# Kernel tuning notes

Measured on AMD Instinct MI355X. Metric: run time of the kernel, lower is better.

The kernel has to match this reference:

```python
import jax, jax.numpy as jnp
import numpy as np

NQ = 8
NL = 6
DIM = 2 ** NQ
C64 = jnp.complex64
I2 = jnp.eye(2, dtype=C64)
PX = jnp.array([[0., 1.], [1., 0.]], dtype=C64)
PY = jnp.array([[0., -1j], [1j, 0.]], dtype=C64)
PZ = jnp.array([[1., 0.], [0., -1.]], dtype=C64)
# sign of Pauli-Z eigenvalue for each computational basis state, wires 0..3 (wire 0 = MSB)
_idx = np.arange(DIM)
_SIGNS = jnp.asarray(np.stack([1.0 - 2.0 * ((_idx >> (NQ - 1 - w)) & 1) for w in range(4)]).astype(np.float32))  # (4, 256)

def _rot(t, P):
    # exp(-i t/2 P) = cos(t/2) I - i sin(t/2) P
    th = t.astype(jnp.float32) / 2
    return jnp.cos(th) * I2 - 1j * jnp.sin(th) * P

def _apply1(st, U, w):
    # apply 2x2 unitary U on wire w; st: (B, 2,2,...,2)
    s = jnp.moveaxis(st, w + 1, -1)
    return jnp.moveaxis(s @ U.T, -1, w + 1)

def _cnot(st, c, t):
    # flip target axis where control bit == 1
    s = jnp.moveaxis(st, (c + 1, t + 1), (1, 2))
    s = jnp.concatenate([s[:, :1], s[:, 1:, ::-1]], axis=1)
    return jnp.moveaxis(s, (1, 2), (c + 1, t + 1))

def _quantum(x, weights):
    B = x.shape[0]
    # AmplitudeEmbedding with normalize=True
    psi = (x / jnp.linalg.norm(x, axis=1, keepdims=True)).astype(C64)
    st = psi.reshape((B,) + (2,) * NQ)
    for l in range(NL):
        lw = weights[l]
        for q in range(NQ):
            st = _apply1(st, _rot(lw[3 * q], PX), q)
            st = _apply1(st, _rot(lw[3 * q + 1], PY), q)
            st = _apply1(st, _rot(lw[3 * q + 2], PZ), q)
        for i in range(NQ - 1):
            st = _cnot(st, i, i + 1)
        st = _cnot(st, NQ - 1, 0)
        for i in range(0, NQ, 2):
            if i + 2 < NQ:
                st = _cnot(st, i, i + 2)
    probs = jnp.abs(st.reshape(B, DIM)) ** 2
    return probs @ _SIGNS.T  # (B, 4) Z expectations on wires 0..3

def _bn(h, g, b):
    # BatchNorm1d, training mode (batch statistics, biased variance)
    m = h.mean(0)
    v = h.var(0)
    return g * (h - m) * jax.lax.rsqrt(v + 1e-5) + b

def _forward(x, q_weights, aW, ab, fW1, fb1, fW2, fb2, cW1, cb1, g1, be1, cW2, cb2, g2, be2, cW3, cb3, cW4, cb4):
    q = _quantum(x, q_weights)                     # (B, 4)
    qf = q @ aW.T + ab                             # quantum_adapter
    cf = jnp.tanh(jax.nn.relu(x @ fW1.T + fb1) @ fW2.T + fb2)  # feature_processor
    h = qf + cf
    h = jax.nn.relu(_bn(h @ cW1.T + cb1, g1, be1))
    h = jax.nn.relu(_bn(h @ cW2.T + cb2, g2, be2))
    h = jax.nn.relu(h @ cW3.T + cb3)
    return jax.nn.sigmoid(h @ cW4.T + cb4)         # (B, 1)

def setup_inputs():
    key = jax.random.key(0)
    ks = jax.random.split(key, 21)
    f32 = jnp.float32
    r = lambda k, shp, s: jax.random.normal(k, shp, dtype=f32) * s
    B = 8192
    return {
        'x': r(ks[0], (B, 256), 1.0),
        'q_weights': r(ks[1], (NL, NQ * 3), 1.0),
        'aW': r(ks[2], (4, 4), 0.5), 'ab': r(ks[3], (4,), 0.1),
        'fW1': r(ks[4], (64, 256), 0.0625), 'fb1': r(ks[5], (64,), 0.05),
        'fW2': r(ks[6], (4, 64), 0.125), 'fb2': r(ks[7], (4,), 0.05),
        'cW1': r(ks[8], (32, 4), 0.5), 'cb1': r(ks[9], (32,), 0.05),
        'g1': 1.0 + r(ks[10], (32,), 0.05), 'be1': r(ks[11], (32,), 0.05),
        'cW2': r(ks[12], (16, 32), 0.18), 'cb2': r(ks[13], (16,), 0.05),
        'g2': 1.0 + r(ks[14], (16,), 0.05), 'be2': r(ks[15], (16,), 0.05),
        'cW3': r(ks[16], (8, 16), 0.25), 'cb3': r(ks[17], (8,), 0.05),
        'cW4': r(ks[18], (1, 8), 0.35), 'cb4': r(ks[19], (1,), 0.05),
    }

def reference(x, q_weights, aW, ab, fW1, fb1, fW2, fb2, cW1, cb1, g1, be1, cW2, cb2, g2, be2, cW3, cb3, cW4, cb4):
    return _forward(x, q_weights, aW, ab, fW1, fb1, fW2, fb2, cW1, cb1, g1, be1, cW2, cb2, g2, be2, cW3, cb3, cW4, cb4)
```

## Files before the change

kernel.cpp:

```cpp
#include <hip/hip_runtime.h>
#include <math.h>

#define INV_B (1.0f / 8192.0f)

typedef float  v2f  __attribute__((ext_vector_type(2)));
typedef _Float16 half8 __attribute__((ext_vector_type(8)));
typedef float  f32x4 __attribute__((ext_vector_type(4)));

struct QTables {
    int xm[6][8];
    int rm[6][8];
    int meas[4];
};
constexpr QTables make_tables() {
    QTables T{};
    int Mrow[8] = {}, Ncol[8] = {};
    for (int b = 0; b < 8; ++b) { Mrow[b] = 1 << b; Ncol[b] = 1 << b; }
    constexpr int bc[11] = {7,6,5,4,3,2,1,0,7,5,3};
    constexpr int bt[11] = {6,5,4,3,2,1,0,7,5,3,1};
    for (int l = 0; l < 6; ++l) {
        for (int w = 0; w < 8; ++w) { T.xm[l][w] = Ncol[7 - w]; T.rm[l][w] = Mrow[7 - w]; }
        for (int k = 0; k < 11; ++k) { Mrow[bt[k]] ^= Mrow[bc[k]]; Ncol[bc[k]] ^= Ncol[bt[k]]; }
    }
    for (int w = 0; w < 4; ++w) T.meas[w] = Mrow[7 - w];
    return T;
}
constexpr QTables TB = make_tables();

template<int ML>
static __device__ __forceinline__ float lanex(float v) {
    if constexpr (ML == 0) { return v; }
    else if constexpr (ML == 1) { return __int_as_float(__builtin_amdgcn_update_dpp(0, __float_as_int(v), 0xB1, 0xF, 0xF, true)); }
    else if constexpr (ML == 2) { return __int_as_float(__builtin_amdgcn_update_dpp(0, __float_as_int(v), 0x4E, 0xF, 0xF, true)); }
    else if constexpr (ML == 3) { return __int_as_float(__builtin_amdgcn_update_dpp(0, __float_as_int(v), 0x1B, 0xF, 0xF, true)); }
    else if constexpr (ML < 32) { return __int_as_float(__builtin_amdgcn_ds_swizzle(__float_as_int(v), 0x1F | (ML << 10))); }
    else { return __shfl_xor(v, ML, 64); }
}

static __device__ __forceinline__ float bsum64(float v) {
    v += lanex<1>(v);  v += lanex<2>(v);
    v += lanex<4>(v);  v += lanex<8>(v);
    v += lanex<16>(v); v += __shfl_xor(v, 32, 64);
    return v;
}

static __device__ __forceinline__ float tanh_fast(float v) {
    const float c = fminf(fmaxf(v, -10.f), 10.f);
    const float e = __expf(2.f * c);
    return (e - 1.f) / (e + 1.f);
}

template<int XM, int RM>
static __device__ __forceinline__ void gate(v2f (&z)[4], const int lane,
                                            const float u00r, const float u00i,
                                            const float u01r, const float u01i) {
    constexpr int ML = XM >> 2, MR = XM & 3;
    constexpr int RL = RM >> 2, RR = RM & 3;
    const int pl = __popc(lane & RL) & 1;
    const float csi0 = pl ? -u00i : u00i;
    const float cpr0 = pl ? -u01r : u01r;
    const float csi1 = -csi0, cpr1 = -cpr0;
    v2f p[4];
    #pragma unroll
    for (int r = 0; r < 4; ++r) {
        p[r].x = lanex<ML>(z[r ^ MR].x);
        p[r].y = lanex<ML>(z[r ^ MR].y);
    }
    #pragma unroll
    for (int r = 0; r < 4; ++r) {
        const int pb = __builtin_popcount(r & RR) & 1;
        const float csi = pb ? csi1 : csi0;
        const float cpr = pb ? cpr1 : cpr0;
        const v2f zs = { -z[r].y, z[r].x };
        const v2f ps = { -p[r].y, p[r].x };
        z[r] = ((u00r * z[r] + csi * zs) + cpr * p[r]) + u01i * ps;
    }
}

#define XS 264
__global__ __launch_bounds__(256) void k_feat(
        const float* __restrict__ x, const float* __restrict__ qw,
        const float* __restrict__ fW1, const float* __restrict__ fb1,
        const float* __restrict__ fW2, const float* __restrict__ fb2,
        float* __restrict__ U, float* __restrict__ cfws, float* __restrict__ accz) {
    const int t = threadIdx.x, b = blockIdx.x;

    if (t < 16) accz[b * 16 + t] = 0.f;
    if (b == 0 && t < 48) {
        const int l = t >> 3, q = t & 7;
        const float* a = qw + l * 24 + q * 3;
        const float h1 = 0.5f * a[0], h2 = 0.5f * a[1], h3 = 0.5f * a[2];
        const float c1 = cosf(h1), s1 = sinf(h1);
        const float c2 = cosf(h2), s2 = sinf(h2);
        const float c3 = cosf(h3), s3 = sinf(h3);
        const float m00r =  c1 * c2, m00i =  s1 * s2;
        const float m01r = -c1 * s2, m01i = -s1 * c2;
        float4 u;
        u.x = m00r * c3 + m00i * s3;  u.y = m00i * c3 - m00r * s3;
        u.z = m01r * c3 + m01i * s3;  u.w = m01i * c3 - m01r * s3;
        ((float4*)U)[t] = u;
    }

    __shared__ _Float16 xl[64 * XS];
    __shared__ _Float16 wl[64 * XS];
    const long r0 = (long)b * 64;
    #pragma unroll
    for (int i = 0; i < 16; ++i) {
        const int idx = i * 256 + t;
        const int row = idx >> 6, c4 = idx & 63;
        const float4 xv = ((const float4*)(x + (r0 + row) * 256))[c4];
        _Float16* d = &xl[row * XS + c4 * 4];
        d[0] = (_Float16)xv.x; d[1] = (_Float16)xv.y;
        d[2] = (_Float16)xv.z; d[3] = (_Float16)xv.w;
        const float4 wv = ((const float4*)(fW1 + (long)row * 256))[c4];
        _Float16* e = &wl[row * XS + c4 * 4];
        e[0] = (_Float16)wv.x; e[1] = (_Float16)wv.y;
        e[2] = (_Float16)wv.z; e[3] = (_Float16)wv.w;
    }
    __syncthreads();

    const int lane = t & 63, w4 = t >> 6;
    const int g = lane >> 4, col = lane & 15;
    const int rloc = w4 * 16 + col;

    half8 bf[8];
    #pragma unroll
    for (int kb = 0; kb < 8; ++kb)
        bf[kb] = *(const half8*)&xl[rloc * XS + kb * 32 + g * 8];

    float accc[4] = {0.f, 0.f, 0.f, 0.f};
    #pragma unroll
    for (int jc = 0; jc < 4; ++jc) {
        f32x4 cv = {0.f, 0.f, 0.f, 0.f};
        #pragma unroll
        for (int kb = 0; kb < 8; ++kb) {
            const half8 af = *(const half8*)&wl[(jc * 16 + col) * XS + kb * 32 + g * 8];
            cv = __builtin_amdgcn_mfma_f32_16x16x32_f16(af, bf[kb], cv, 0, 0, 0);
        }
        #pragma unroll
        for (int r = 0; r < 4; ++r) {
            const int j = jc * 16 + g * 4 + r;
            const float z = fmaxf(cv[r] + fb1[j], 0.f);
            #pragma unroll
            for (int c = 0; c < 4; ++c) accc[c] += z * fW2[c * 64 + j];
        }
    }
    #pragma unroll
    for (int c = 0; c < 4; ++c) {
        accc[c] += __shfl_xor(accc[c], 16, 64);
        accc[c] += __shfl_xor(accc[c], 32, 64);
    }
    if (g == 0) {
        float4 o;
        o.x = tanh_fast(accc[0] + fb2[0]);
        o.y = tanh_fast(accc[1] + fb2[1]);
        o.z = tanh_fast(accc[2] + fb2[2]);
        o.w = tanh_fast(accc[3] + fb2[3]);
        ((float4*)cfws)[r0 + w4 * 16 + col] = o;
    }
}

__global__ __launch_bounds__(256) void k_main(
        const float* __restrict__ x, const float* __restrict__ U,
        const float* __restrict__ cfws,
        const float* __restrict__ aW, const float* __restrict__ ab,
        float* __restrict__ hws, float* __restrict__ acc1) {
    const int t = threadIdx.x, lane = t & 63, wv = t >> 6;
    const int b = blockIdx.x;
    const int row = b * 4 + wv;

    const float4 xr = ((const float4*)(x + (long)row * 256))[lane];

    v2f z[4] = { {xr.x, 0.f}, {xr.y, 0.f}, {xr.z, 0.f}, {xr.w, 0.f} };
    const float4* U4 = (const float4*)U;

#define GATE(L, W) { const float4 u = U4[(L) * 8 + (W)]; \
                     gate<TB.xm[L][W], TB.rm[L][W]>(z, lane, u.x, u.y, u.z, u.w); }
#define LAYER(L) GATE(L,0) GATE(L,1) GATE(L,2) GATE(L,3) GATE(L,4) GATE(L,5) GATE(L,6) GATE(L,7)
    LAYER(0) LAYER(1) LAYER(2) LAYER(3) LAYER(4) LAYER(5)
#undef LAYER
#undef GATE

    float pv[4];
    #pragma unroll
    for (int r = 0; r < 4; ++r) pv[r] = z[r].x * z[r].x + z[r].y * z[r].y;
    float S = pv[0] + pv[1] + pv[2] + pv[3];
    float qs[4];
    #pragma unroll
    for (int w = 0; w < 4; ++w) {
        const int mm = TB.meas[w];
        const int plm = __popc(lane & (mm >> 2)) & 1;
        float s = 0.f;
        #pragma unroll
        for (int r = 0; r < 4; ++r) {
            const int sgn = plm ^ (__builtin_popcount(r & (mm & 3)) & 1);
            s += sgn ? -pv[r] : pv[r];
        }
        qs[w] = s;
    }
    S = bsum64(S);
    const float inv = 1.0f / S;
    float qe[4];
    #pragma unroll
    for (int w = 0; w < 4; ++w) qe[w] = bsum64(qs[w]) * inv;

    const float4 cfv = ((const float4*)cfws)[row];
    const float cf[4] = {cfv.x, cfv.y, cfv.z, cfv.w};
    float h[4];
    #pragma unroll
    for (int k = 0; k < 4; ++k) {
        float s = ab[k] + cf[k];
        #pragma unroll
        for (int j = 0; j < 4; ++j) s += aW[k * 4 + j] * qe[j];
        h[k] = s;
    }
    if (lane == 0)
        ((float4*)hws)[row] = make_float4(h[0], h[1], h[2], h[3]);

    __shared__ float wsum[4][20];
    if (lane == 0) {
        #pragma unroll
        for (int k = 0; k < 4; ++k) wsum[wv][k] = h[k];
        #pragma unroll
        for (int j = 0; j < 4; ++j)
            #pragma unroll
            for (int k = 0; k < 4; ++k) wsum[wv][4 + j * 4 + k] = h[j] * h[k];
    }
    __syncthreads();
    if (t < 20)
        atomicAdd(acc1 + (b & 31) * 20 + t,
                  wsum[0][t] + wsum[1][t] + wsum[2][t] + wsum[3][t]);
}

__global__ __launch_bounds__(64) void k_mid(
        const float* __restrict__ hws, const float* __restrict__ acc1,
        const float* __restrict__ cW1, const float* __restrict__ cb1,
        const float* __restrict__ g1, const float* __restrict__ be1,
        const float* __restrict__ cW2, const float* __restrict__ cb2,
        float* __restrict__ z2ws, float* __restrict__ acc2) {
    const int t = threadIdx.x;
    __shared__ float sA[20];
    __shared__ float m1s[32], is1[32];
    if (t < 20) {
        float s = 0.f;
        for (int sl = 0; sl < 32; ++sl) s += acc1[sl * 20 + t];
        sA[t] = s;
    }
    __syncthreads();
    if (t < 32) {
        float mu[4], w[4];
        #pragma unroll
        for (int k = 0; k < 4; ++k) mu[k] = sA[k] * INV_B;
        float m = cb1[t];
        #pragma unroll
        for (int k = 0; k < 4; ++k) { w[k] = cW1[t * 4 + k]; m += w[k] * mu[k]; }
        float var = 0.f;
        #pragma unroll
        for (int a2 = 0; a2 < 4; ++a2)
            #pragma unroll
            for (int b2 = 0; b2 < 4; ++b2)
                var += w[a2] * w[b2] * (sA[4 + a2 * 4 + b2] * INV_B - mu[a2] * mu[b2]);
        m1s[t] = m;
        is1[t] = 1.0f / sqrtf(var + 1e-5f);
    }
    __syncthreads();

    const long e = (long)blockIdx.x * 64 + t;
    const float4 h4 = ((const float4*)hws)[e];
    const float h[4] = {h4.x, h4.y, h4.z, h4.w};
    float a1[32];
    #pragma unroll
    for (int j = 0; j < 32; ++j) {
        float zz = cb1[j];
        #pragma unroll
        for (int k = 0; k < 4; ++k) zz += cW1[j * 4 + k] * h[k];
        a1[j] = fmaxf((zz - m1s[j]) * is1[j] * g1[j] + be1[j], 0.f);
    }
    float z2[16];
    #pragma unroll
    for (int k = 0; k < 16; ++k) {
        float s = cb2[k];
        #pragma unroll
        for (int j = 0; j < 32; ++j) s += cW2[k * 32 + j] * a1[j];
        z2[k] = s;
    }
    float4* zp = (float4*)(z2ws + e * 16);
    zp[0] = make_float4(z2[0], z2[1], z2[2], z2[3]);
    zp[1] = make_float4(z2[4], z2[5], z2[6], z2[7]);
    zp[2] = make_float4(z2[8], z2[9], z2[10], z2[11]);
    zp[3] = make_float4(z2[12], z2[13], z2[14], z2[15]);

    float sv[16], sq[16];
    #pragma unroll
    for (int k = 0; k < 16; ++k) { sv[k] = z2[k]; sq[k] = z2[k] * z2[k]; }
    #pragma unroll
    for (int m = 1; m < 64; m <<= 1) {
        #pragma unroll
        for (int k = 0; k < 16; ++k) {
            sv[k] += __shfl_xor(sv[k], m, 64);
            sq[k] += __shfl_xor(sq[k], m, 64);
        }
    }
    if (t == 0) {
        float* dst = acc2 + (blockIdx.x & 31) * 32;
        #pragma unroll
        for (int k = 0; k < 16; ++k) atomicAdd(dst + k, sv[k]);
        #pragma unroll
        for (int k = 0; k < 16; ++k) atomicAdd(dst + 16 + k, sq[k]);
    }
}

__global__ __launch_bounds__(64) void k_out(
        const float* __restrict__ z2ws, const float* __restrict__ acc2,
        const float* __restrict__ g2, const float* __restrict__ be2,
        const float* __restrict__ cW3, const float* __restrict__ cb3,
        const float* __restrict__ cW4, const float* __restrict__ cb4,
        float* __restrict__ out) {
    const int t = threadIdx.x;
    __shared__ float sB[32];
    __shared__ float m2s[16], is2[16];
    if (t < 32) {
        float s = 0.f;
        for (int sl = 0; sl < 32; ++sl) s += acc2[sl * 32 + t];
        sB[t] = s;
    }
    __syncthreads();
    if (t < 16) {
        const float m = sB[t] * INV_B;
        const float var = sB[16 + t] * INV_B - m * m;
        m2s[t] = m;
        is2[t] = 1.0f / sqrtf(var + 1e-5f);
    }
    __syncthreads();

    const long e = (long)blockIdx.x * 64 + t;
    const float4* zp = (const float4*)(z2ws + e * 16);
    const float4 v0 = zp[0], v1 = zp[1], v2 = zp[2], v3 = zp[3];
    const float z2[16] = {v0.x, v0.y, v0.z, v0.w, v1.x, v1.y, v1.z, v1.w,
                          v2.x, v2.y, v2.z, v2.w, v3.x, v3.y, v3.z, v3.w};
    float a2[16];
    #pragma unroll
    for (int k = 0; k < 16; ++k)
        a2[k] = fmaxf((z2[k] - m2s[k]) * is2[k] * g2[k] + be2[k], 0.f);
    float z3[8];
    #pragma unroll
    for (int j = 0; j < 8; ++j) {
        float s = cb3[j];
        #pragma unroll
        for (int k = 0; k < 16; ++k) s += cW3[j * 16 + k] * a2[k];
        z3[j] = fmaxf(s, 0.f);
    }
    float y = cb4[0];
    #pragma unroll
    for (int j = 0; j < 8; ++j) y += cW4[j] * z3[j];
    out[e] = 1.0f / (1.0f + expf(-y));
}

extern "C" void kernel_launch(void* const* d_in, const int* in_sizes, int n_in,
                              void* d_out, int out_size, void* d_ws, size_t ws_size,
                              hipStream_t stream) {
    (void)in_sizes; (void)n_in; (void)out_size; (void)ws_size;
    const float* x   = (const float*)d_in[0];
    const float* qw  = (const float*)d_in[1];
    const float* aW  = (const float*)d_in[2];
    const float* ab  = (const float*)d_in[3];
    const float* fW1 = (const float*)d_in[4];
    const float* fb1 = (const float*)d_in[5];
    const float* fW2 = (const float*)d_in[6];
    const float* fb2 = (const float*)d_in[7];
    const float* cW1 = (const float*)d_in[8];
    const float* cb1 = (const float*)d_in[9];
    const float* g1  = (const float*)d_in[10];
    const float* be1 = (const float*)d_in[11];
    const float* cW2 = (const float*)d_in[12];
    const float* cb2 = (const float*)d_in[13];
    const float* g2  = (const float*)d_in[14];
    const float* be2 = (const float*)d_in[15];
    const float* cW3 = (const float*)d_in[16];
    const float* cb3 = (const float*)d_in[17];
    const float* cW4 = (const float*)d_in[18];
    const float* cb4 = (const float*)d_in[19];

    float* ws   = (float*)d_ws;
    float* acc1 = ws;
    float* acc2 = ws + 1024;
    float* U    = ws + 2048;
    float* cfws = ws + 4096;
    float* hws  = ws + 40960;
    float* z2ws = ws + 81920;

    k_feat<<<128, 256, 0, stream>>>(x, qw, fW1, fb1, fW2, fb2, U, cfws, ws);
    k_main<<<2048, 256, 0, stream>>>(x, U, cfws, aW, ab, hws, acc1);
    k_mid <<<128, 64, 0, stream>>>(hws, acc1, cW1, cb1, g1, be1, cW2, cb2, z2ws, acc2);
    k_out <<<128, 64, 0, stream>>>(z2ws, acc2, g2, be2, cW3, cb3, cW4, cb4, (float*)d_out);
}
```

Measured before the change: 148.1 us.

## Process two state rows per wave and fuse the BatchNorm tail kernels with a grid barrier

The quantum-simulation kernel now carries two batch rows per wavefront, eight complex registers per lane, so each gate's cross-lane exchanges and FMAs for two independent states interleave. This adds instruction-level parallelism and halves the grid. The last two small kernels are merged into one, using an atomic counter spin barrier across the 128 blocks to get the second BatchNorm statistics. That drops a launch and the z2 workspace round-trip, but relies on all blocks being co-resident.

Result: slower. 151.7 us (+2.4%).

```diff
diff --git a/kernel.cpp b/kernel.cpp
--- a/kernel.cpp
+++ b/kernel.cpp
@@ -51,29 +51,30 @@
 }
 
 template<int XM, int RM>
-static __device__ __forceinline__ void gate(v2f (&z)[4], const int lane,
-                                            const float u00r, const float u00i,
-                                            const float u01r, const float u01i) {
+static __device__ __forceinline__ void gate2(v2f (&z)[8], const int lane,
+                                             const float u00r, const float u00i,
+                                             const float u01r, const float u01i) {
     constexpr int ML = XM >> 2, MR = XM & 3;
     constexpr int RL = RM >> 2, RR = RM & 3;
     const int pl = __popc(lane & RL) & 1;
     const float csi0 = pl ? -u00i : u00i;
     const float cpr0 = pl ? -u01r : u01r;
     const float csi1 = -csi0, cpr1 = -cpr0;
-    v2f p[4];
-    #pragma unroll
-    for (int r = 0; r < 4; ++r) {
-        p[r].x = lanex<ML>(z[r ^ MR].x);
-        p[r].y = lanex<ML>(z[r ^ MR].y);
-    }
-    #pragma unroll
-    for (int r = 0; r < 4; ++r) {
-        const int pb = __builtin_popcount(r & RR) & 1;
+    v2f p[8];
+    #pragma unroll
+    for (int rr = 0; rr < 8; ++rr) {
+        const int src = (rr & 4) | ((rr & 3) ^ MR);
+        p[rr].x = lanex<ML>(z[src].x);
+        p[rr].y = lanex<ML>(z[src].y);
+    }
+    #pragma unroll
+    for (int rr = 0; rr < 8; ++rr) {
+        const int pb = __builtin_popcount(rr & RR) & 1;
         const float csi = pb ? csi1 : csi0;
         const float cpr = pb ? cpr1 : cpr0;
-        const v2f zs = { -z[r].y, z[r].x };
-        const v2f ps = { -p[r].y, p[r].x };
-        z[r] = ((u00r * z[r] + csi * zs) + cpr * p[r]) + u01i * ps;
+        const v2f zs = { -z[rr].y, z[rr].x };
+        const v2f ps = { -p[rr].y, p[rr].x };
+        z[rr] = ((u00r * z[rr] + csi * zs) + cpr * p[rr]) + u01i * ps;
     }
 }
 
@@ -167,77 +168,94 @@
         float* __restrict__ hws, float* __restrict__ acc1) {
     const int t = threadIdx.x, lane = t & 63, wv = t >> 6;
     const int b = blockIdx.x;
-    const int row = b * 4 + wv;
-
-    const float4 xr = ((const float4*)(x + (long)row * 256))[lane];
-
-    v2f z[4] = { {xr.x, 0.f}, {xr.y, 0.f}, {xr.z, 0.f}, {xr.w, 0.f} };
+    const int rowA = b * 8 + wv * 2, rowB = rowA + 1;
+
+    const float4 xa = ((const float4*)(x + (long)rowA * 256))[lane];
+    const float4 xb = ((const float4*)(x + (long)rowB * 256))[lane];
+    const float4 cfa = ((const float4*)cfws)[rowA];
+    const float4 cfb = ((const float4*)cfws)[rowB];
+
+    v2f z[8] = { {xa.x, 0.f}, {xa.y, 0.f}, {xa.z, 0.f}, {xa.w, 0.f},
+                 {xb.x, 0.f}, {xb.y, 0.f}, {xb.z, 0.f}, {xb.w, 0.f} };
     const float4* U4 = (const float4*)U;
 
 #define GATE(L, W) { const float4 u = U4[(L) * 8 + (W)]; \
-                     gate<TB.xm[L][W], TB.rm[L][W]>(z, lane, u.x, u.y, u.z, u.w); }
+                     gate2<TB.xm[L][W], TB.rm[L][W]>(z, lane, u.x, u.y, u.z, u.w); }
 #define LAYER(L) GATE(L,0) GATE(L,1) GATE(L,2) GATE(L,3) GATE(L,4) GATE(L,5) GATE(L,6) GATE(L,7)
     LAYER(0) LAYER(1) LAYER(2) LAYER(3) LAYER(4) LAYER(5)
 #undef LAYER
 #undef GATE
 
-    float pv[4];
-    #pragma unroll
-    for (int r = 0; r < 4; ++r) pv[r] = z[r].x * z[r].x + z[r].y * z[r].y;
-    float S = pv[0] + pv[1] + pv[2] + pv[3];
-    float qs[4];
-    #pragma unroll
-    for (int w = 0; w < 4; ++w) {
-        const int mm = TB.meas[w];
-        const int plm = __popc(lane & (mm >> 2)) & 1;
-        float s = 0.f;
+    float hA[4], hB[4];
+    #pragma unroll
+    for (int half = 0; half < 2; ++half) {
+        float pv[4];
         #pragma unroll
         for (int r = 0; r < 4; ++r) {
-            const int sgn = plm ^ (__builtin_popcount(r & (mm & 3)) & 1);
-            s += sgn ? -pv[r] : pv[r];
-        }
-        qs[w] = s;
-    }
-    S = bsum64(S);
-    const float inv = 1.0f / S;
-    float qe[4];
-    #pragma unroll
-    for (int w = 0; w < 4; ++w) qe[w] = bsum64(qs[w]) * inv;
-
-    const float4 cfv = ((const float4*)cfws)[row];
-    const float cf[4] = {cfv.x, cfv.y, cfv.z, cfv.w};
-    float h[4];
-    #pragma unroll
-    for (int k = 0; k < 4; ++k) {
-        float s = ab[k] + cf[k];
-        #pragma unroll
-        for (int j = 0; j < 4; ++j) s += aW[k * 4 + j] * qe[j];
-        h[k] = s;
-    }
-    if (lane == 0)
-        ((float4*)hws)[row] = make_float4(h[0], h[1], h[2], h[3]);
-
-    __shared__ float wsum[4][20];
+            const v2f zz = z[half * 4 + r];
+            pv[r] = zz.x * zz.x + zz.y * zz.y;
+        }
+        float S = pv[0] + pv[1] + pv[2] + pv[3];
+        float qs[4];
+        #pragma unroll
+        for (int w = 0; w < 4; ++w) {
+            const int mm = TB.meas[w];
+            const int plm = __popc(lane & (mm >> 2)) & 1;
+            float s = 0.f;
+            #pragma unroll
+            for (int r = 0; r < 4; ++r) {
+                const int sgn = plm ^ (__builtin_popcount(r & (mm & 3)) & 1);
+                s += sgn ? -pv[r] : pv[r];
+            }
+            qs[w] = s;
+        }
+        S = bsum64(S);
+        const float inv = 1.0f / S;
+        float qe[4];
+        #pragma unroll
+        for (int w = 0; w < 4; ++w) qe[w] = bsum64(qs[w]) * inv;
+
+        const float4 cfv = half ? cfb : cfa;
+        const float cf[4] = {cfv.x, cfv.y, cfv.z, cfv.w};
+        float* h = half ? hB : hA;
+        #pragma unroll
+        for (int k = 0; k < 4; ++k) {
+            float s = ab[k] + cf[k];
+            #pragma unroll
+            for (int j = 0; j < 4; ++j) s += aW[k * 4 + j] * qe[j];
+            h[k] = s;
+        }
+    }
     if (lane == 0) {
-        #pragma unroll
-        for (int k = 0; k < 4; ++k) wsum[wv][k] = h[k];
-        #pragma unroll
-        for (int j = 0; j < 4; ++j)
-            #pragma unroll
-            for (int k = 0; k < 4; ++k) wsum[wv][4 + j * 4 + k] = h[j] * h[k];
-    }
-    __syncthreads();
-    if (t < 20)
-        atomicAdd(acc1 + (b & 31) * 20 + t,
-                  wsum[0][t] + wsum[1][t] + wsum[2][t] + wsum[3][t]);
-}
-
-__global__ __launch_bounds__(64) void k_mid(
+        ((float4*)hws)[rowA] = make_float4(hA[0], hA[1], hA[2], hA[3]);
+        ((float4*)hws)[rowB] = make_float4(hB[0], hB[1], hB[2], hB[3]);
+    }
+
+    __shared__ float wsum[8][20];
+    if (lane < 20) {
+        const int j = (lane - 4) >> 2, k = (lane - 4) & 3;
+        wsum[wv * 2 + 0][lane] = (lane < 4) ? hA[lane] : hA[j] * hA[k];
+        wsum[wv * 2 + 1][lane] = (lane < 4) ? hB[lane] : hB[j] * hB[k];
+    }
+    __syncthreads();
+    if (t < 20) {
+        float v = 0.f;
+        #pragma unroll
+        for (int i = 0; i < 8; ++i) v += wsum[i][t];
+        atomicAdd(acc1 + (b & 31) * 20 + t, v);
+    }
+}
+
+__global__ __launch_bounds__(64) void k_tail(
         const float* __restrict__ hws, const float* __restrict__ acc1,
         const float* __restrict__ cW1, const float* __restrict__ cb1,
         const float* __restrict__ g1, const float* __restrict__ be1,
         const float* __restrict__ cW2, const float* __restrict__ cb2,
-        float* __restrict__ z2ws, float* __restrict__ acc2) {
+        const float* __restrict__ g2, const float* __restrict__ be2,
+        const float* __restrict__ cW3, const float* __restrict__ cb3,
+        const float* __restrict__ cW4, const float* __restrict__ cb4,
+        float* __restrict__ acc2, int* __restrict__ cnt,
+        float* __restrict__ out) {
     const int t = threadIdx.x;
     __shared__ float sA[20];
     __shared__ float m1s[32], is1[32];
@@ -284,11 +302,6 @@
         for (int j = 0; j < 32; ++j) s += cW2[k * 32 + j] * a1[j];
         z2[k] = s;
     }
-    float4* zp = (float4*)(z2ws + e * 16);
-    zp[0] = make_float4(z2[0], z2[1], z2[2], z2[3]);
-    zp[1] = make_float4(z2[4], z2[5], z2[6], z2[7]);
-    zp[2] = make_float4(z2[8], z2[9], z2[10], z2[11]);
-    zp[3] = make_float4(z2[12], z2[13], z2[14], z2[15]);
 
     float sv[16], sq[16];
     #pragma unroll
@@ -302,42 +315,37 @@
         }
     }
     if (t == 0) {
-        float* dst = acc2 + (blockIdx.x & 31) * 32;
+        float* dst = acc2 + ((int)blockIdx.x & 31) * 32;
         #pragma unroll
         for (int k = 0; k < 16; ++k) atomicAdd(dst + k, sv[k]);
         #pragma unroll
         for (int k = 0; k < 16; ++k) atomicAdd(dst + 16 + k, sq[k]);
-    }
-}
-
-__global__ __launch_bounds__(64) void k_out(
-        const float* __restrict__ z2ws, const float* __restrict__ acc2,
-        const float* __restrict__ g2, const float* __restrict__ be2,
-        const float* __restrict__ cW3, const float* __restrict__ cb3,
-        const float* __restrict__ cW4, const float* __restrict__ cb4,
-        float* __restrict__ out) {
-    const int t = threadIdx.x;
-    __shared__ float sB[32];
+        __threadfence();
+        __hip_atomic_fetch_add(cnt, 1, __ATOMIC_ACQ_REL, __HIP_MEMORY_SCOPE_AGENT);
+        while (__hip_atomic_load(cnt, __ATOMIC_ACQUIRE, __HIP_MEMORY_SCOPE_AGENT)
+               < (int)gridDim.x) { __builtin_amdgcn_s_sleep(2); }
+    }
+    __syncthreads();
+
     __shared__ float m2s[16], is2[16];
     if (t < 32) {
         float s = 0.f;
-        for (int sl = 0; sl < 32; ++sl) s += acc2[sl * 32 + t];
+        for (int sl = 0; sl < 32; ++sl)
+            s += __hip_atomic_load(acc2 + sl * 32 + t, __ATOMIC_RELAXED,
+                                   __HIP_MEMORY_SCOPE_AGENT);
+        sA[t < 20 ? t : 0] = 0.f;
+        if (t < 16) {  }
+        __shared__ float sB[32];
         sB[t] = s;
-    }
-    __syncthreads();
-    if (t < 16) {
-        const float m = sB[t] * INV_B;
-        const float var = sB[16 + t] * INV_B - m * m;
-        m2s[t] = m;
-        is2[t] = 1.0f / sqrtf(var + 1e-5f);
-    }
-    __syncthreads();
-
-    const long e = (long)blockIdx.x * 64 + t;
-    const float4* zp = (const float4*)(z2ws + e * 16);
-    const float4 v0 = zp[0], v1 = zp[1], v2 = zp[2], v3 = zp[3];
-    const float z2[16] = {v0.x, v0.y, v0.z, v0.w, v1.x, v1.y, v1.z, v1.w,
-                          v2.x, v2.y, v2.z, v2.w, v3.x, v3.y, v3.z, v3.w};
+        __syncthreads();
+        if (t < 16) {
+            const float m = sB[t] * INV_B;
+            m2s[t] = m;
+            is2[t] = 1.0f / sqrtf(sB[16 + t] * INV_B - m * m + 1e-5f);
+        }
+    }
+    __syncthreads();
+
     float a2[16];
     #pragma unroll
     for (int k = 0; k < 16; ++k)
@@ -383,14 +391,15 @@
 
     float* ws   = (float*)d_ws;
     float* acc1 = ws;
+    int*   cnt  = (int*)(ws + 640);
     float* acc2 = ws + 1024;
     float* U    = ws + 2048;
     float* cfws = ws + 4096;
     float* hws  = ws + 40960;
-    float* z2ws = ws + 81920;
 
     k_feat<<<128, 256, 0, stream>>>(x, qw, fW1, fb1, fW2, fb2, U, cfws, ws);
-    k_main<<<2048, 256, 0, stream>>>(x, U, cfws, aW, ab, hws, acc1);
-    k_mid <<<128, 64, 0, stream>>>(hws, acc1, cW1, cb1, g1, be1, cW2, cb2, z2ws, acc2);
-    k_out <<<128, 64, 0, stream>>>(z2ws, acc2, g2, be2, cW3, cb3, cW4, cb4, (float*)d_out);
-}
+    k_main<<<1024, 256, 0, stream>>>(x, U, cfws, aW, ab, hws, acc1);
+    k_tail<<<128, 64, 0, stream>>>(hws, acc1, cW1, cb1, g1, be1, cW2, cb2,
+                                   g2, be2, cW3, cb3, cW4, cb4, acc2, cnt,
+                                   (float*)d_out);
+}
```

## Precompute circuit unitary and apply it to all rows as an fp16 MFMA GEMM

Applied to the files above, without the earlier changes.

Rather than simulating the 48 gates on every batch row, extra blocks in the first kernel build the full 256x256 circuit unitary once by pushing each basis vector through the gates, and store it in fp16. The main kernel then multiplies the fp16 input rows by the real and imaginary parts of this unitary using MFMA and reduces probabilities with sign masks to get the Z expectations. This swaps a long per-row chain of cross-lane shuffles for dense matrix-core work. It adds fp16 rounding of the unitary and the inputs, which may cost accuracy.

Result: faster. 137.7 us (-7.0%).

```diff
diff --git a/kernel.cpp b/kernel.cpp
--- a/kernel.cpp
+++ b/kernel.cpp
@@ -37,13 +37,6 @@
     else { return __shfl_xor(v, ML, 64); }
 }
 
-static __device__ __forceinline__ float bsum64(float v) {
-    v += lanex<1>(v);  v += lanex<2>(v);
-    v += lanex<4>(v);  v += lanex<8>(v);
-    v += lanex<16>(v); v += __shfl_xor(v, 32, 64);
-    return v;
-}
-
 static __device__ __forceinline__ float tanh_fast(float v) {
     const float c = fminf(fmaxf(v, -10.f), 10.f);
     const float e = __expf(2.f * c);
@@ -78,28 +71,55 @@
 }
 
 #define XS 264
-__global__ __launch_bounds__(256) void k_feat(
+__global__ __launch_bounds__(256) void k_pre(
         const float* __restrict__ x, const float* __restrict__ qw,
         const float* __restrict__ fW1, const float* __restrict__ fb1,
         const float* __restrict__ fW2, const float* __restrict__ fb2,
-        float* __restrict__ U, float* __restrict__ cfws, float* __restrict__ accz) {
+        _Float16* __restrict__ Wt, float* __restrict__ cfws,
+        float* __restrict__ accz) {
     const int t = threadIdx.x, b = blockIdx.x;
 
+    if (b >= 128) {
+        __shared__ float4 Us[48];
+        if (t < 48) {
+            const int l = t >> 3, q = t & 7;
+            const float* a = qw + l * 24 + q * 3;
+            const float h1 = 0.5f * a[0], h2 = 0.5f * a[1], h3 = 0.5f * a[2];
+            const float c1 = cosf(h1), s1 = sinf(h1);
+            const float c2 = cosf(h2), s2 = sinf(h2);
+            const float c3 = cosf(h3), s3 = sinf(h3);
+            const float m00r =  c1 * c2, m00i =  s1 * s2;
+            const float m01r = -c1 * s2, m01i = -s1 * c2;
+            float4 u;
+            u.x = m00r * c3 + m00i * s3;  u.y = m00i * c3 - m00r * s3;
+            u.z = m01r * c3 + m01i * s3;  u.w = m01i * c3 - m01r * s3;
+            Us[t] = u;
+        }
+        __syncthreads();
+        const int lane = t & 63, wv = t >> 6;
+        const int k = (b - 128) * 4 + wv;
+        v2f z[4];
+        #pragma unroll
+        for (int r = 0; r < 4; ++r) {
+            z[r].x = (4 * lane + r == k) ? 1.f : 0.f;
+            z[r].y = 0.f;
+        }
+#define GATE(L, W) { const float4 u = Us[(L) * 8 + (W)]; \
+                     gate<TB.xm[L][W], TB.rm[L][W]>(z, lane, u.x, u.y, u.z, u.w); }
+#define LAYER(L) GATE(L,0) GATE(L,1) GATE(L,2) GATE(L,3) GATE(L,4) GATE(L,5) GATE(L,6) GATE(L,7)
+        LAYER(0) LAYER(1) LAYER(2) LAYER(3) LAYER(4) LAYER(5)
+#undef LAYER
+#undef GATE
+        #pragma unroll
+        for (int r = 0; r < 4; ++r) {
+            const int i = 4 * lane + r;
+            Wt[(long)i * 256 + k]         = (_Float16)z[r].x;
+            Wt[(long)(256 + i) * 256 + k] = (_Float16)z[r].y;
+        }
+        return;
+    }
+
     if (t < 16) accz[b * 16 + t] = 0.f;
-    if (b == 0 && t < 48) {
-        const int l = t >> 3, q = t & 7;
-        const float* a = qw + l * 24 + q * 3;
-        const float h1 = 0.5f * a[0], h2 = 0.5f * a[1], h3 = 0.5f * a[2];
-        const float c1 = cosf(h1), s1 = sinf(h1);
-        const float c2 = cosf(h2), s2 = sinf(h2);
-        const float c3 = cosf(h3), s3 = sinf(h3);
-        const float m00r =  c1 * c2, m00i =  s1 * s2;
-        const float m01r = -c1 * s2, m01i = -s1 * c2;
-        float4 u;
-        u.x = m00r * c3 + m00i * s3;  u.y = m00i * c3 - m00r * s3;
-        u.z = m01r * c3 + m01i * s3;  u.w = m01i * c3 - m01r * s3;
-        ((float4*)U)[t] = u;
-    }
 
     __shared__ _Float16 xl[64 * XS];
     __shared__ _Float16 wl[64 * XS];
@@ -112,10 +132,10 @@
         _Float16* d = &xl[row * XS + c4 * 4];
         d[0] = (_Float16)xv.x; d[1] = (_Float16)xv.y;
         d[2] = (_Float16)xv.z; d[3] = (_Float16)xv.w;
-        const float4 wv = ((const float4*)(fW1 + (long)row * 256))[c4];
+        const float4 wv2 = ((const float4*)(fW1 + (long)row * 256))[c4];
         _Float16* e = &wl[row * XS + c4 * 4];
-        e[0] = (_Float16)wv.x; e[1] = (_Float16)wv.y;
-        e[2] = (_Float16)wv.z; e[3] = (_Float16)wv.w;
+        e[0] = (_Float16)wv2.x; e[1] = (_Float16)wv2.y;
+        e[2] = (_Float16)wv2.z; e[3] = (_Float16)wv2.w;
     }
     __syncthreads();
 
@@ -160,76 +180,118 @@
     }
 }
 
-__global__ __launch_bounds__(256) void k_main(
-        const float* __restrict__ x, const float* __restrict__ U,
+__global__ __launch_bounds__(128) void k_gemm(
+        const float* __restrict__ x, const _Float16* __restrict__ Wt,
         const float* __restrict__ cfws,
         const float* __restrict__ aW, const float* __restrict__ ab,
         float* __restrict__ hws, float* __restrict__ acc1) {
-    const int t = threadIdx.x, lane = t & 63, wv = t >> 6;
-    const int b = blockIdx.x;
-    const int row = b * 4 + wv;
-
-    const float4 xr = ((const float4*)(x + (long)row * 256))[lane];
-
-    v2f z[4] = { {xr.x, 0.f}, {xr.y, 0.f}, {xr.z, 0.f}, {xr.w, 0.f} };
-    const float4* U4 = (const float4*)U;
-
-#define GATE(L, W) { const float4 u = U4[(L) * 8 + (W)]; \
-                     gate<TB.xm[L][W], TB.rm[L][W]>(z, lane, u.x, u.y, u.z, u.w); }
-#define LAYER(L) GATE(L,0) GATE(L,1) GATE(L,2) GATE(L,3) GATE(L,4) GATE(L,5) GATE(L,6) GATE(L,7)
-    LAYER(0) LAYER(1) LAYER(2) LAYER(3) LAYER(4) LAYER(5)
-#undef LAYER
-#undef GATE
-
-    float pv[4];
-    #pragma unroll
-    for (int r = 0; r < 4; ++r) pv[r] = z[r].x * z[r].x + z[r].y * z[r].y;
-    float S = pv[0] + pv[1] + pv[2] + pv[3];
-    float qs[4];
-    #pragma unroll
-    for (int w = 0; w < 4; ++w) {
-        const int mm = TB.meas[w];
-        const int plm = __popc(lane & (mm >> 2)) & 1;
-        float s = 0.f;
+    const int t = threadIdx.x;
+    const int lane = t & 63, w = t >> 6;
+    const int col = lane & 15, quad = lane >> 4;
+    const int R0 = blockIdx.x * 32;
+
+    __shared__ _Float16 xa[32 * XS];
+    #pragma unroll
+    for (int i = 0; i < 16; ++i) {
+        const int idx = i * 128 + t;
+        const int row = idx >> 6, c4 = idx & 63;
+        const float4 xv = ((const float4*)(x + (long)(R0 + row) * 256))[c4];
+        _Float16* d = &xa[row * XS + c4 * 4];
+        d[0] = (_Float16)xv.x; d[1] = (_Float16)xv.y;
+        d[2] = (_Float16)xv.z; d[3] = (_Float16)xv.w;
+    }
+    __syncthreads();
+
+    half8 af[8];
+    #pragma unroll
+    for (int kb = 0; kb < 8; ++kb)
+        af[kb] = *(const half8*)&xa[(w * 16 + col) * XS + kb * 32 + quad * 8];
+
+    int slm[4];
+    #pragma unroll
+    for (int mw = 0; mw < 4; ++mw) slm[mw] = __popc(col & TB.meas[mw]) & 1;
+
+    float sS[4] = {0.f, 0.f, 0.f, 0.f};
+    float sq[4][4] = {{0.f}};
+    const _Float16* bre = Wt + (long)col * 256;
+    const _Float16* bim = Wt + (long)(256 + col) * 256;
+
+    #pragma unroll
+    for (int c = 0; c < 16; ++c) {
+        f32x4 cr0 = {0.f,0.f,0.f,0.f}, cr1 = {0.f,0.f,0.f,0.f};
+        f32x4 ci0 = {0.f,0.f,0.f,0.f}, ci1 = {0.f,0.f,0.f,0.f};
+        const long rowoff = (long)(c * 16) * 256 + quad * 8;
+        #pragma unroll
+        for (int kb = 0; kb < 4; ++kb) {
+            const half8 br = *(const half8*)(bre + rowoff + kb * 32);
+            cr0 = __builtin_amdgcn_mfma_f32_16x16x32_f16(af[kb], br, cr0, 0, 0, 0);
+            const half8 bi = *(const half8*)(bim + rowoff + kb * 32);
+            ci0 = __builtin_amdgcn_mfma_f32_16x16x32_f16(af[kb], bi, ci0, 0, 0, 0);
+            const half8 br2 = *(const half8*)(bre + rowoff + (kb + 4) * 32);
+            cr1 = __builtin_amdgcn_mfma_f32_16x16x32_f16(af[kb + 4], br2, cr1, 0, 0, 0);
+            const half8 bi2 = *(const half8*)(bim + rowoff + (kb + 4) * 32);
+            ci1 = __builtin_amdgcn_mfma_f32_16x16x32_f16(af[kb + 4], bi2, ci1, 0, 0, 0);
+        }
+        float sgn[4];
+        #pragma unroll
+        for (int mw = 0; mw < 4; ++mw) {
+            const int scw = __builtin_popcount((c * 16) & TB.meas[mw]) & 1;
+            sgn[mw] = (slm[mw] ^ scw) ? -1.f : 1.f;
+        }
         #pragma unroll
         for (int r = 0; r < 4; ++r) {
-            const int sgn = plm ^ (__builtin_popcount(r & (mm & 3)) & 1);
-            s += sgn ? -pv[r] : pv[r];
-        }
-        qs[w] = s;
-    }
-    S = bsum64(S);
-    const float inv = 1.0f / S;
-    float qe[4];
-    #pragma unroll
-    for (int w = 0; w < 4; ++w) qe[w] = bsum64(qs[w]) * inv;
-
-    const float4 cfv = ((const float4*)cfws)[row];
-    const float cf[4] = {cfv.x, cfv.y, cfv.z, cfv.w};
-    float h[4];
-    #pragma unroll
-    for (int k = 0; k < 4; ++k) {
-        float s = ab[k] + cf[k];
-        #pragma unroll
-        for (int j = 0; j < 4; ++j) s += aW[k * 4 + j] * qe[j];
-        h[k] = s;
-    }
-    if (lane == 0)
-        ((float4*)hws)[row] = make_float4(h[0], h[1], h[2], h[3]);
-
-    __shared__ float wsum[4][20];
-    if (lane == 0) {
-        #pragma unroll
-        for (int k = 0; k < 4; ++k) wsum[wv][k] = h[k];
-        #pragma unroll
-        for (int j = 0; j < 4; ++j)
+            const float re = cr0[r] + cr1[r], im = ci0[r] + ci1[r];
+            const float p = re * re + im * im;
+            sS[r] += p;
             #pragma unroll
-            for (int k = 0; k < 4; ++k) wsum[wv][4 + j * 4 + k] = h[j] * h[k];
-    }
-    __syncthreads();
-    if (t < 20)
-        atomicAdd(acc1 + (b & 31) * 20 + t,
-                  wsum[0][t] + wsum[1][t] + wsum[2][t] + wsum[3][t]);
+            for (int mw = 0; mw < 4; ++mw) sq[mw][r] = fmaf(sgn[mw], p, sq[mw][r]);
+        }
+    }
+
+    #pragma unroll
+    for (int r = 0; r < 4; ++r) {
+        sS[r] += lanex<1>(sS[r]); sS[r] += lanex<2>(sS[r]);
+        sS[r] += lanex<4>(sS[r]); sS[r] += lanex<8>(sS[r]);
+        #pragma unroll
+        for (int mw = 0; mw < 4; ++mw) {
+            sq[mw][r] += lanex<1>(sq[mw][r]); sq[mw][r] += lanex<2>(sq[mw][r]);
+            sq[mw][r] += lanex<4>(sq[mw][r]); sq[mw][r] += lanex<8>(sq[mw][r]);
+        }
+    }
+
+    __shared__ float hb[32][4];
+    if (col == 0) {
+        #pragma unroll
+        for (int r = 0; r < 4; ++r) {
+            const int mloc = w * 16 + quad * 4 + r;
+            const int row = R0 + mloc;
+            const float inv = 1.0f / sS[r];
+            float qe[4];
+            #pragma unroll
+            for (int mw = 0; mw < 4; ++mw) qe[mw] = sq[mw][r] * inv;
+            const float4 cfv = ((const float4*)cfws)[row];
+            const float cf[4] = {cfv.x, cfv.y, cfv.z, cfv.w};
+            float h[4];
+            #pragma unroll
+            for (int kk = 0; kk < 4; ++kk) {
+                float s = ab[kk] + cf[kk];
+                #pragma unroll
+                for (int j = 0; j < 4; ++j) s += aW[kk * 4 + j] * qe[j];
+                h[kk] = s;
+            }
+            ((float4*)hws)[row] = make_float4(h[0], h[1], h[2], h[3]);
+            hb[mloc][0] = h[0]; hb[mloc][1] = h[1];
+            hb[mloc][2] = h[2]; hb[mloc][3] = h[3];
+        }
+    }
+    __syncthreads();
+    if (t < 20) {
+        const int j = (t - 4) >> 2, kk = (t - 4) & 3;
+        float v = 0.f;
+        for (int rr = 0; rr < 32; ++rr)
+            v += (t < 4) ? hb[rr][t] : hb[rr][j] * hb[rr][kk];
+        atomicAdd(acc1 + (blockIdx.x & 31) * 20 + t, v);
+    }
 }
 
 __global__ __launch_bounds__(64) void k_mid(
@@ -290,23 +352,23 @@
     zp[2] = make_float4(z2[8], z2[9], z2[10], z2[11]);
     zp[3] = make_float4(z2[12], z2[13], z2[14], z2[15]);
 
-    float sv[16], sq[16];
-    #pragma unroll
-    for (int k = 0; k < 16; ++k) { sv[k] = z2[k]; sq[k] = z2[k] * z2[k]; }
+    float sv[16], sq2[16];
+    #pragma unroll
+    for (int k = 0; k < 16; ++k) { sv[k] = z2[k]; sq2[k] = z2[k] * z2[k]; }
     #pragma unroll
     for (int m = 1; m < 64; m <<= 1) {
         #pragma unroll
         for (int k = 0; k < 16; ++k) {
             sv[k] += __shfl_xor(sv[k], m, 64);
-            sq[k] += __shfl_xor(sq[k], m, 64);
+            sq2[k] += __shfl_xor(sq2[k], m, 64);
         }
     }
     if (t == 0) {
-        float* dst = acc2 + (blockIdx.x & 31) * 32;
+        float* dst = acc2 + ((int)blockIdx.x & 31) * 32;
         #pragma unroll
         for (int k = 0; k < 16; ++k) atomicAdd(dst + k, sv[k]);
         #pragma unroll
-        for (int k = 0; k < 16; ++k) atomicAdd(dst + 16 + k, sq[k]);
+        for (int k = 0; k < 16; ++k) atomicAdd(dst + 16 + k, sq2[k]);
     }
 }
 
@@ -384,13 +446,13 @@
     float* ws   = (float*)d_ws;
     float* acc1 = ws;
     float* acc2 = ws + 1024;
-    float* U    = ws + 2048;
     float* cfws = ws + 4096;
     float* hws  = ws + 40960;
     float* z2ws = ws + 81920;
-
-    k_feat<<<128, 256, 0, stream>>>(x, qw, fW1, fb1, fW2, fb2, U, cfws, ws);
-    k_main<<<2048, 256, 0, stream>>>(x, U, cfws, aW, ab, hws, acc1);
+    _Float16* Wt = (_Float16*)(ws + 215040);
+
+    k_pre <<<192, 256, 0, stream>>>(x, qw, fW1, fb1, fW2, fb2, Wt, cfws, ws);
+    k_gemm<<<256, 128, 0, stream>>>(x, Wt, cfws, aW, ab, hws, acc1);
     k_mid <<<128, 64, 0, stream>>>(hws, acc1, cW1, cb1, g1, be1, cW2, cb2, z2ws, acc2);
     k_out <<<128, 64, 0, stream>>>(z2ws, acc2, g2, be2, cW3, cb3, cW4, cb4, (float*)d_out);
 }
```
